# Performance work log

Hardware: AMD Instinct MI355X
Metric: run time of the kernel (lower is better)

The kernel has to match this reference:

```python
import jax, jax.numpy as jnp
import numpy as np

EPS = 1e-5
K_NUM, EDGE_TYPE = 5, 2  # k_num = A_fixed_partitions(3) + edge_type(2)


def _bn(x, gamma, beta):
    # training-mode BatchNorm2d: batch stats over (N, T, V) per channel
    m = jnp.mean(x, axis=(0, 2, 3), keepdims=True)
    v = jnp.var(x, axis=(0, 2, 3), keepdims=True)
    return (x - m) * jax.lax.rsqrt(v + EPS) * gamma[None, :, None, None] + beta[None, :, None, None]


def setup_inputs() -> dict:
    key = jax.random.key(0)
    ks = jax.random.split(key, 6)
    N, C, T, V = 32, 64, 300, 25
    Cout, Kt = 64, 9
    x = jax.random.normal(ks[0], (N, C, T, V), jnp.float32)
    A = jax.random.uniform(ks[1], (K_NUM - EDGE_TYPE, V, V), jnp.float32) / V  # fixed adjacency (already scaled by edge_importance)
    B = jax.random.uniform(ks[2], (N, EDGE_TYPE, V, V), jnp.float32) / V      # per-sample adaptive adjacency A_act
    lamda_act = jnp.full((1,), 0.5, jnp.float32)
    conv_w = jax.random.normal(ks[3], (Cout * K_NUM, C), jnp.float32) * (1.0 / np.sqrt(C))  # 1x1 conv weight
    conv_b = jnp.zeros((Cout * K_NUM,), jnp.float32)
    bn1_g = jnp.ones((Cout,), jnp.float32)
    bn1_b = jnp.zeros((Cout,), jnp.float32)
    tcn_w = jax.random.normal(ks[4], (Cout, Cout, Kt, 1), jnp.float32) * (1.0 / np.sqrt(Cout * Kt))
    tcn_b = jnp.zeros((Cout,), jnp.float32)
    bn2_g = jnp.ones((Cout,), jnp.float32)
    bn2_b = jnp.zeros((Cout,), jnp.float32)
    return dict(x=x, A=A, B=B, lamda_act=lamda_act, conv_w=conv_w, conv_b=conv_b,
                bn1_g=bn1_g, bn1_b=bn1_b, tcn_w=tcn_w, tcn_b=tcn_b, bn2_g=bn2_g, bn2_b=bn2_b)


def reference(x, A, B, lamda_act, conv_w, conv_b, bn1_g, bn1_b, tcn_w, tcn_b, bn2_g, bn2_b):
    n, c, t, v = x.shape
    res = x  # identity residual (in_ch == out_ch, stride 1)
    # SpatialGcn: 1x1 conv (pure channel GEMM) -> split -> dual einsum graph conv
    y = jnp.einsum('nctv,oc->notv', x, conv_w) + conv_b[None, :, None, None]  # (n, K*Cout, t, v)
    cout = y.shape[1] // K_NUM
    y = y.reshape(n, K_NUM, cout, t, v)
    x1 = jnp.einsum('nkctv,kvw->nctw', y[:, :K_NUM - EDGE_TYPE], A)   # fixed adjacency
    x2 = jnp.einsum('nkctv,nkvw->nctw', y[:, K_NUM - EDGE_TYPE:], B)  # adaptive adjacency
    g = x1 + x2 * lamda_act[0]
    # tcn: BN -> ReLU -> temporal conv (9,1) pad (4,0) -> BN -> Dropout(0)=identity
    h = jax.nn.relu(_bn(g, bn1_g, bn1_b))
    h = jax.lax.conv_general_dilated(h, tcn_w, window_strides=(1, 1),
                                     padding=((4, 4), (0, 0)),
                                     dimension_numbers=('NCHW', 'OIHW', 'NCHW'))
    h = h + tcn_b[None, :, None, None]
    h = _bn(h, bn2_g, bn2_b)
    return jax.nn.relu(h + res)
```

## Files before the change

### kernel.cpp

```cpp
#include <hip/hip_runtime.h>
#include <hip/hip_bf16.h>

#define N_  32
#define C_  64
#define T_  300
#define V_  25
#define TV  (T_*V_)
#define CTV (C_*TV)
#define NELEM (N_*CTV)
#define CNTF 240000.0f

typedef float f32x4 __attribute__((ext_vector_type(4)));
typedef short bf16x8 __attribute__((ext_vector_type(8)));
typedef short s4v __attribute__((ext_vector_type(4)));
typedef short s8v __attribute__((ext_vector_type(8)));

__device__ __forceinline__ unsigned short f2bf(float f) {
    unsigned u = __float_as_uint(f);
    unsigned r = u + 0x7fffu + ((u >> 16) & 1u);
    return (unsigned short)(r >> 16);
}
__device__ __forceinline__ float bf2f(unsigned short u) {
    return __uint_as_float(((unsigned)u) << 16);
}

__global__ __launch_bounds__(256) void k_prep(
    const float* __restrict__ conv_w, const float* __restrict__ tw,
    unsigned short* __restrict__ w2b, unsigned short* __restrict__ twb)
{
    int tid = blockIdx.x*256 + threadIdx.x;
    for (int e = tid; e < 20480; e += 8192) {
        int ks = e >> 11, c = (e >> 5) & 63, kk = e & 31;
        w2b[e] = f2bf(conv_w[(((ks>>1)*64 + c)*64) + (ks&1)*32 + kk]);
    }
    for (int e = tid; e < 36864; e += 8192) {
        int gi = e >> 11, c = (e >> 5) & 63, kk = e & 31;
        int dt = gi >> 1, ks = gi & 1;
        twb[e] = f2bf(tw[(c*64 + 32*ks + kk)*9 + dt]);
    }
}

__global__ __launch_bounds__(256) void k_gcn(
    const float* __restrict__ x, const float* __restrict__ A,
    const float* __restrict__ B, const float* __restrict__ lamda,
    const unsigned short* __restrict__ w2b, const float* __restrict__ conv_b,
    unsigned short* __restrict__ gout, float* __restrict__ stats3)
{
    __shared__ unsigned short ash[5*32*40];
    __shared__ unsigned short zsh[32*328];
    __shared__ unsigned short gsh[25*68];
    __shared__ float csum[160];
    __shared__ float sbc[320];

    const int tb = blockIdx.x, n = blockIdx.y;
    const int t0 = tb*10;
    const int tid = threadIdx.x;
    const int lane = tid & 63, wv = tid >> 6;
    const int lg = lane >> 4, lr = lane & 15;
    const int crow = lr + 16*wv;
    const int cbase = 16*wv + 4*lg;

    bf16x8 wfrag[10];
    #pragma unroll
    for (int ks = 0; ks < 10; ++ks)
        wfrag[ks] = *(const bf16x8*)&w2b[(ks*64 + crow)*32 + 8*lg];

    const float lam = lamda[0];
    for (int e = tid; e < 6400; e += 256) {
        int k = e / 1280, r = e % 1280, w = r / 40, v = r % 40;
        float val = 0.f;
        if (w < 25 && v < 25)
            val = (k < 3) ? A[k*625 + v*25 + w]
                          : lam * B[((n<<1) + (k-3))*625 + v*25 + w];
        ash[e] = f2bf(val);
    }
    for (int e = tid; e < 320; e += 256) sbc[e] = conv_b[e];
    __syncthreads();
    for (int e = tid; e < 160; e += 256) {
        int k = e / 32, w = e % 32;
        float s = 0.f;
        for (int v = 0; v < 25; ++v) s += bf2f(ash[k*1280 + w*40 + v]);
        csum[e] = s;
    }
    __syncthreads();

    float bs0[4], bs1[4];
    #pragma unroll
    for (int r = 0; r < 4; ++r) {
        float s0 = 0.f, s1 = 0.f;
        #pragma unroll
        for (int k = 0; k < 5; ++k) {
            float cb = sbc[k*64 + cbase + r];
            s0 += cb * csum[k*32 + lr];
            s1 += cb * csum[k*32 + lr + 16];
        }
        bs0[r] = s0; bs1[r] = s1;
    }

    float sacc[4] = {0,0,0,0}, qacc[4] = {0,0,0,0};

    const float* xrow = x + n*CTV + crow*TV + t0*V_;
    float xf[8];
    #pragma unroll
    for (int i = 0; i < 8; ++i) { int v = 8*lg + i; xf[i] = (v < 25) ? xrow[v] : 0.f; }

    for (int tl = 0; tl < 10; ++tl) {
        bf16x8 xfrag;
        #pragma unroll
        for (int i = 0; i < 8; ++i) xfrag[i] = (short)f2bf(xf[i]);
        if (tl < 9) {
            const float* xn = xrow + (tl+1)*V_;
            #pragma unroll
            for (int i = 0; i < 8; ++i) { int v = 8*lg + i; xf[i] = (v < 25) ? xn[v] : 0.f; }
        }
        #pragma unroll
        for (int k = 0; k < 5; ++k)
        #pragma unroll
        for (int nt = 0; nt < 2; ++nt) {
            bf16x8 bfrag = *(const bf16x8*)&ash[k*1280 + (lr + 16*nt)*40 + 8*lg];
            f32x4 z = {0.f,0.f,0.f,0.f};
            z = __builtin_amdgcn_mfma_f32_16x16x32_bf16(xfrag, bfrag, z, 0, 0, 0);
            s4v z4;
            #pragma unroll
            for (int r = 0; r < 4; ++r) z4[r] = (short)f2bf(z[r]);
            *(s4v*)&zsh[(lr + 16*nt)*328 + k*64 + 16*wv + 4*lg] = z4;
        }
        __syncthreads();
        f32x4 acc0 = {0.f,0.f,0.f,0.f}, acc1 = {0.f,0.f,0.f,0.f};
        #pragma unroll
        for (int ks = 0; ks < 10; ++ks) {
            bf16x8 b0 = *(const bf16x8*)&zsh[lr*328 + 32*ks + 8*lg];
            bf16x8 b1 = *(const bf16x8*)&zsh[(lr+16)*328 + 32*ks + 8*lg];
            acc0 = __builtin_amdgcn_mfma_f32_16x16x32_bf16(wfrag[ks], b0, acc0, 0, 0, 0);
            acc1 = __builtin_amdgcn_mfma_f32_16x16x32_bf16(wfrag[ks], b1, acc1, 0, 0, 0);
        }
        s4v g0, g1;
        #pragma unroll
        for (int r = 0; r < 4; ++r) {
            float v0 = acc0[r] + bs0[r];
            float v1 = acc1[r] + bs1[r];
            g0[r] = (short)f2bf(v0); g1[r] = (short)f2bf(v1);
            sacc[r] += v0 + (lr < 9 ? v1 : 0.f);
            qacc[r] += v0*v0 + (lr < 9 ? v1*v1 : 0.f);
        }
        *(s4v*)&gsh[lr*68 + cbase] = g0;
        if (lr < 9) *(s4v*)&gsh[(lr+16)*68 + cbase] = g1;
        __syncthreads();
        unsigned short* grow = gout + (size_t)(n*300 + t0 + tl)*1600;
        for (int e = tid; e < 1600; e += 256)
            grow[e] = gsh[(e >> 6)*68 + (e & 63)];
    }

    #pragma unroll
    for (int r = 0; r < 4; ++r) {
        float s = sacc[r], q = qacc[r];
        s += __shfl_xor(s, 1); s += __shfl_xor(s, 2);
        s += __shfl_xor(s, 4); s += __shfl_xor(s, 8);
        q += __shfl_xor(q, 1); q += __shfl_xor(q, 2);
        q += __shfl_xor(q, 4); q += __shfl_xor(q, 8);
        if (lr == 0) {
            stats3[(n*30 + tb)*128 + cbase + r] = s;
            stats3[(n*30 + tb)*128 + 64 + cbase + r] = q;
        }
    }
}

__global__ __launch_bounds__(256) void k_fin(
    const float* __restrict__ src, int count, float* __restrict__ sbo,
    const float* __restrict__ gma, const float* __restrict__ bta)
{
    const int c = blockIdx.x, tid = threadIdx.x;
    float s = 0.f, q = 0.f;
    for (int b = tid; b < count; b += 256) {
        s += src[b*128 + c];
        q += src[b*128 + 64 + c];
    }
    #pragma unroll
    for (int m = 1; m < 64; m <<= 1) { s += __shfl_xor(s, m); q += __shfl_xor(q, m); }
    __shared__ float rs[4], rq[4];
    if ((tid & 63) == 0) { rs[tid>>6] = s; rq[tid>>6] = q; }
    __syncthreads();
    if (tid == 0) {
        s = rs[0]+rs[1]+rs[2]+rs[3]; q = rq[0]+rq[1]+rq[2]+rq[3];
        float mean = s / CNTF, var = q / CNTF - mean*mean;
        float sc = gma[c] * rsqrtf(var + 1e-5f);
        sbo[c] = sc;
        sbo[64 + c] = bta[c] - mean*sc;
    }
}

__global__ __launch_bounds__(256) void k_tcn(
    const unsigned short* __restrict__ gin, const float* __restrict__ sb,
    const unsigned short* __restrict__ twb, const float* __restrict__ tb,
    unsigned short* __restrict__ hout, float* __restrict__ stats4)
{
    __shared__ unsigned short pT[16*25*72];
    __shared__ float sbs[128];

    const int n = blockIdx.y, tt = blockIdx.x, t0 = tt*8;
    const int tid = threadIdx.x;
    const int lane = tid & 63, wv = tid >> 6;
    const int lg = lane >> 4, lr = lane & 15;
    const int c = lr + 16*wv;
    const int cbase = 16*wv + 4*lg;

    bf16x8 af[18];
    #pragma unroll
    for (int gi = 0; gi < 18; ++gi)
        af[gi] = *(const bf16x8*)&twb[(gi*64 + c)*32 + 8*lg];

    for (int e = tid; e < 128; e += 256) sbs[e] = sb[e];
    __syncthreads();

    for (int e8 = tid; e8 < 3200; e8 += 256) {
        int tl = e8 / 200, r = e8 % 200, w = r >> 3, i8 = (r & 7) * 8;
        int tg = t0 - 4 + tl;
        s8v val8 = {0,0,0,0,0,0,0,0};
        if (tg >= 0 && tg < 300) {
            s8v raw = *(const s8v*)&gin[(size_t)((n*300 + tg)*25 + w)*64 + i8];
            #pragma unroll
            for (int j = 0; j < 8; ++j) {
                float f = fmaf(bf2f((unsigned short)raw[j]), sbs[i8+j], sbs[64+i8+j]);
                val8[j] = (short)f2bf(fmaxf(f, 0.f));
            }
        }
        *(s8v*)&pT[(tl*25 + w)*72 + i8] = val8;
    }
    __syncthreads();

    f32x4 acc[13];
    #pragma unroll
    for (int nt = 0; nt < 13; ++nt) {
        int col = lr + 16*nt; if (col > 199) col = 199;
        int tlo = (col*41) >> 10;
        int w = col - tlo*25;
        f32x4 a = {0.f,0.f,0.f,0.f};
        #pragma unroll
        for (int dt = 0; dt < 9; ++dt) {
            int rowbase = ((tlo + dt)*25 + w)*72 + 8*lg;
            bf16x8 b0 = *(const bf16x8*)&pT[rowbase];
            bf16x8 b1 = *(const bf16x8*)&pT[rowbase + 32];
            a = __builtin_amdgcn_mfma_f32_16x16x32_bf16(af[dt*2],     b0, a, 0, 0, 0);
            a = __builtin_amdgcn_mfma_f32_16x16x32_bf16(af[dt*2 + 1], b1, a, 0, 0, 0);
        }
        acc[nt] = a;
    }

    const int lim = min(200, (300 - t0)*25);
    float tbc[4];
    #pragma unroll
    for (int r = 0; r < 4; ++r) tbc[r] = tb[cbase + r];

    float sacc[4] = {0,0,0,0}, qacc[4] = {0,0,0,0};
    #pragma unroll
    for (int nt = 0; nt < 13; ++nt) {
        int col = lr + 16*nt;
        if (col < lim) {
            #pragma unroll
            for (int r = 0; r < 4; ++r) {
                float v = acc[nt][r] + tbc[r];
                sacc[r] += v; qacc[r] += v*v;
            }
        }
    }
    #pragma unroll
    for (int r = 0; r < 4; ++r) {
        float s = sacc[r], q = qacc[r];
        s += __shfl_xor(s, 1); s += __shfl_xor(s, 2);
        s += __shfl_xor(s, 4); s += __shfl_xor(s, 8);
        q += __shfl_xor(q, 1); q += __shfl_xor(q, 2);
        q += __shfl_xor(q, 4); q += __shfl_xor(q, 8);
        if (lr == 0) {
            stats4[(n*38 + tt)*128 + cbase + r] = s;
            stats4[(n*38 + tt)*128 + 64 + cbase + r] = q;
        }
    }

    __syncthreads();
    float* hbuf = (float*)pT;
    #pragma unroll
    for (int nt = 0; nt < 13; ++nt) {
        int col = lr + 16*nt;
        if (col < 200) {
            #pragma unroll
            for (int r = 0; r < 4; ++r)
                hbuf[(cbase + r)*200 + col] = acc[nt][r] + tbc[r];
        }
    }
    __syncthreads();
    for (int e2 = tid; e2 < 6400; e2 += 256) {
        int row = e2 / 100, c2 = (e2 - row*100)*2;
        if (c2 < lim) {
            float f0 = hbuf[row*200 + c2], f1 = hbuf[row*200 + c2 + 1];
            ushort2 o; o.x = f2bf(f0); o.y = f2bf(f1);
            *(ushort2*)&hout[((size_t)(n*64 + row)*300 + t0)*25 + c2] = o;
        }
    }
}

__global__ __launch_bounds__(256) void k_out(
    const unsigned short* __restrict__ h, const float* __restrict__ x,
    const float* __restrict__ sb, float* __restrict__ out)
{
    int i4 = blockIdx.x * 256 + threadIdx.x;
    if (i4 >= NELEM/4) return;
    int c = ((i4*4) / TV) & 63;
    float s2 = sb[128 + c], b2 = sb[192 + c];
    s4v hv = *(const s4v*)&h[i4*4];
    float4 xv = ((const float4*)x)[i4];
    float4 o;
    o.x = fmaxf(fmaf(bf2f((unsigned short)hv[0]), s2, b2) + xv.x, 0.f);
    o.y = fmaxf(fmaf(bf2f((unsigned short)hv[1]), s2, b2) + xv.y, 0.f);
    o.z = fmaxf(fmaf(bf2f((unsigned short)hv[2]), s2, b2) + xv.z, 0.f);
    o.w = fmaxf(fmaf(bf2f((unsigned short)hv[3]), s2, b2) + xv.w, 0.f);
    ((float4*)out)[i4] = o;
}

extern "C" void kernel_launch(void* const* d_in, const int* in_sizes, int n_in,
                              void* d_out, int out_size, void* d_ws, size_t ws_size,
                              hipStream_t stream)
{
    const float* x      = (const float*)d_in[0];
    const float* A      = (const float*)d_in[1];
    const float* B      = (const float*)d_in[2];
    const float* lamda  = (const float*)d_in[3];
    const float* conv_w = (const float*)d_in[4];
    const float* conv_b = (const float*)d_in[5];
    const float* bn1_g  = (const float*)d_in[6];
    const float* bn1_b  = (const float*)d_in[7];
    const float* tcn_w  = (const float*)d_in[8];
    const float* tcn_b  = (const float*)d_in[9];
    const float* bn2_g  = (const float*)d_in[10];
    const float* bn2_b  = (const float*)d_in[11];

    unsigned short* g = (unsigned short*)d_ws;
    unsigned short* h = g + NELEM;
    float* stats3 = (float*)(h + NELEM);
    float* stats4 = stats3 + 960*128;
    float* sb     = stats4 + 1216*128;
    unsigned short* w2b = (unsigned short*)(sb + 256);
    unsigned short* twb = w2b + 20480;

    k_prep<<<32, 256, 0, stream>>>(conv_w, tcn_w, w2b, twb);
    k_gcn<<<dim3(30, N_), 256, 0, stream>>>(x, A, B, lamda, w2b, conv_b, g, stats3);
    k_fin<<<64, 256, 0, stream>>>(stats3, 960, sb, bn1_g, bn1_b);
    k_tcn<<<dim3(38, N_), 256, 0, stream>>>(g, sb, twb, tcn_b, h, stats4);
    k_fin<<<64, 256, 0, stream>>>(stats4, 1216, sb + 128, bn2_g, bn2_b);
    k_out<<<NELEM/4/256, 256, 0, stream>>>(h, x, sb, (float*)d_out);
}
```

Measured before the change: 144.8 us.

## Split TCN input staging into two channel halves to shrink LDS footprint

The temporal conv kernel now stages the BN+ReLU'd input tile in two 32-channel halves, using a 40-short row stride instead of 72. LDS drops from about 57KB to 32KB, which should allow more blocks per CU. The output staging buffer now holds bf16 and is written back with 4-wide stores instead of fp32 pairs. The cost is an extra pair of barriers and a second load pass that cannot overlap with the MFMA work.

```diff
diff --git a/kernel.cpp b/kernel.cpp
--- a/kernel.cpp
+++ b/kernel.cpp
@@ -194,7 +194,7 @@
     const unsigned short* __restrict__ twb, const float* __restrict__ tb,
     unsigned short* __restrict__ hout, float* __restrict__ stats4)
 {
-    __shared__ unsigned short pT[16*25*72];
+    __shared__ unsigned short pT[400*40];
     __shared__ float sbs[128];
 
     const int n = blockIdx.y, tt = blockIdx.x, t0 = tt*8;
@@ -210,40 +210,39 @@
         af[gi] = *(const bf16x8*)&twb[(gi*64 + c)*32 + 8*lg];
 
     for (int e = tid; e < 128; e += 256) sbs[e] = sb[e];
-    __syncthreads();
-
-    for (int e8 = tid; e8 < 3200; e8 += 256) {
-        int tl = e8 / 200, r = e8 % 200, w = r >> 3, i8 = (r & 7) * 8;
-        int tg = t0 - 4 + tl;
-        s8v val8 = {0,0,0,0,0,0,0,0};
-        if (tg >= 0 && tg < 300) {
-            s8v raw = *(const s8v*)&gin[(size_t)((n*300 + tg)*25 + w)*64 + i8];
-            #pragma unroll
-            for (int j = 0; j < 8; ++j) {
-                float f = fmaf(bf2f((unsigned short)raw[j]), sbs[i8+j], sbs[64+i8+j]);
-                val8[j] = (short)f2bf(fmaxf(f, 0.f));
+
+    f32x4 acc[13];
+    #pragma unroll
+    for (int nt = 0; nt < 13; ++nt) acc[nt] = (f32x4){0.f,0.f,0.f,0.f};
+
+    for (int ks = 0; ks < 2; ++ks) {
+        __syncthreads();
+        for (int e8 = tid; e8 < 1600; e8 += 256) {
+            int tl = e8 / 100, r = e8 % 100, w = r >> 2, ch = r & 3;
+            int tg = t0 - 4 + tl;
+            int i8 = 32*ks + ch*8;
+            s8v val8 = {0,0,0,0,0,0,0,0};
+            if (tg >= 0 && tg < 300) {
+                s8v raw = *(const s8v*)&gin[(size_t)((n*300 + tg)*25 + w)*64 + i8];
+                #pragma unroll
+                for (int j = 0; j < 8; ++j) {
+                    float f = fmaf(bf2f((unsigned short)raw[j]), sbs[i8+j], sbs[64+i8+j]);
+                    val8[j] = (short)f2bf(fmaxf(f, 0.f));
+                }
             }
-        }
-        *(s8v*)&pT[(tl*25 + w)*72 + i8] = val8;
-    }
-    __syncthreads();
-
-    f32x4 acc[13];
-    #pragma unroll
-    for (int nt = 0; nt < 13; ++nt) {
-        int col = lr + 16*nt; if (col > 199) col = 199;
-        int tlo = (col*41) >> 10;
-        int w = col - tlo*25;
-        f32x4 a = {0.f,0.f,0.f,0.f};
-        #pragma unroll
-        for (int dt = 0; dt < 9; ++dt) {
-            int rowbase = ((tlo + dt)*25 + w)*72 + 8*lg;
-            bf16x8 b0 = *(const bf16x8*)&pT[rowbase];
-            bf16x8 b1 = *(const bf16x8*)&pT[rowbase + 32];
-            a = __builtin_amdgcn_mfma_f32_16x16x32_bf16(af[dt*2],     b0, a, 0, 0, 0);
-            a = __builtin_amdgcn_mfma_f32_16x16x32_bf16(af[dt*2 + 1], b1, a, 0, 0, 0);
-        }
-        acc[nt] = a;
+            *(s8v*)&pT[(tl*25 + w)*40 + ch*8] = val8;
+        }
+        __syncthreads();
+
+        #pragma unroll
+        for (int nt = 0; nt < 13; ++nt) {
+            int col = lr + 16*nt; if (col > 199) col = 199;
+            #pragma unroll
+            for (int dt = 0; dt < 9; ++dt) {
+                bf16x8 b = *(const bf16x8*)&pT[(col + 25*dt)*40 + 8*lg];
+                acc[nt] = __builtin_amdgcn_mfma_f32_16x16x32_bf16(af[dt*2 + ks], b, acc[nt], 0, 0, 0);
+            }
+        }
     }
 
     const int lim = min(200, (300 - t0)*25);
@@ -277,23 +276,22 @@
     }
 
     __syncthreads();
-    float* hbuf = (float*)pT;
+    unsigned short* hbuf = pT;
     #pragma unroll
     for (int nt = 0; nt < 13; ++nt) {
         int col = lr + 16*nt;
         if (col < 200) {
             #pragma unroll
             for (int r = 0; r < 4; ++r)
-                hbuf[(cbase + r)*200 + col] = acc[nt][r] + tbc[r];
-        }
-    }
-    __syncthreads();
-    for (int e2 = tid; e2 < 6400; e2 += 256) {
-        int row = e2 / 100, c2 = (e2 - row*100)*2;
-        if (c2 < lim) {
-            float f0 = hbuf[row*200 + c2], f1 = hbuf[row*200 + c2 + 1];
-            ushort2 o; o.x = f2bf(f0); o.y = f2bf(f1);
-            *(ushort2*)&hout[((size_t)(n*64 + row)*300 + t0)*25 + c2] = o;
+                hbuf[(cbase + r)*200 + col] = f2bf(acc[nt][r] + tbc[r]);
+        }
+    }
+    __syncthreads();
+    for (int e = tid; e < 3200; e += 256) {
+        int row = e / 50, c4 = (e % 50)*4;
+        if (c4 < lim) {
+            s4v o = *(const s4v*)&hbuf[row*200 + c4];
+            *(s4v*)&hout[((size_t)(n*64 + row)*300 + t0)*25 + c4] = o;
         }
     }
 }
```

New measurement: 144.4 us. About the same (-0.3%).
